# Performance work log

Measured on AMD Instinct MI355X. Metric: run time of the kernel, lower is better.

Reference implementation:

```python
import jax, jax.numpy as jnp
import numpy as np
import math

N_HEADS = 16

def setup_inputs() -> dict:
    key = jax.random.key(0)
    k1, k2, k3 = jax.random.split(key, 3)
    B, S, D = 2, 2048, 1024
    x = jax.random.normal(k1, (B, S, D), dtype=jnp.float32)
    qkv = 0.01 * jax.random.normal(k2, (3 * D, D), dtype=jnp.float32)
    wo = 0.01 * jax.random.normal(k3, (D, D), dtype=jnp.float32)
    return {"x": x, "qkv": qkv, "wo": wo}

def reference(x, qkv, wo):
    B, S, D = x.shape
    H = N_HEADS
    dh = D // H
    QKV = x @ qkv.T                      # [B,S,3D]
    Q, K, V = jnp.split(QKV, 3, axis=-1)
    q = Q.reshape(B, S, H, dh).transpose(0, 2, 1, 3)  # [B,H,S,dh]
    k = K.reshape(B, S, H, dh).transpose(0, 2, 1, 3)
    v = V.reshape(B, S, H, dh).transpose(0, 2, 1, 3)
    scores = jnp.einsum('bhqd,bhkd->bhqk', q, k) / math.sqrt(float(dh))
    # Faithful to original: multiply by lower-triangular mask, then set
    # exact zeros to -inf (masked positions become 0 then -inf).
    mask = jnp.tril(jnp.ones((S, S), dtype=scores.dtype))
    scores = scores * mask[None, None, :, :]
    scores = jnp.where(scores == 0, -jnp.inf, scores)
    attn = jax.nn.softmax(scores, axis=-1)
    out = jnp.einsum('bhqk,bhkd->bhqd', attn, v)       # [B,H,S,dh]
    out = out.transpose(0, 2, 1, 3).reshape(B, S, D)
    return out @ wo.T
```

## Files before the change

kernel.cpp:

```cpp
#include <hip/hip_runtime.h>

typedef unsigned short u16;
typedef unsigned int u32;
typedef __bf16 bf16x8 __attribute__((ext_vector_type(8)));
typedef float f32x4 __attribute__((ext_vector_type(4)));
typedef u16 u16x4 __attribute__((ext_vector_type(4)));
typedef u16 u16x8 __attribute__((ext_vector_type(8)));

#define GL2LDS16(g, l)                                                         \
    __builtin_amdgcn_global_load_lds(                                          \
        (__attribute__((address_space(1))) const void*)(g),                    \
        (__attribute__((address_space(3))) void*)(l), 16, 0, 0)

#define SYNC_VM(n) asm volatile("s_waitcnt vmcnt(" #n ")\ns_barrier" ::: "memory")
#define BAR()      asm volatile("s_barrier" ::: "memory")
#define BAR_DS()   asm volatile("s_waitcnt lgkmcnt(0)\ns_barrier" ::: "memory")

__device__ __forceinline__ u16 f2bf(float f) {
    union { float f; u32 u; } x; x.f = f;
    u32 r = x.u + 0x7FFFu + ((x.u >> 16) & 1u);
    return (u16)(r >> 16);
}

__device__ __forceinline__ u32 pack2bf(float f0, float f1) {
    union { float f; u32 u; } a, b;
    a.f = f0; b.f = f1;
    return __builtin_amdgcn_perm(b.u + 0x8000u, a.u + 0x8000u, 0x07060302u);
}

__device__ __forceinline__ float fast_exp2(float x) {
    float r;
    asm("v_exp_f32 %0, %1" : "=v"(r) : "v"(x));
    return r;
}

__device__ __forceinline__ bf16x8 scale_frag(bf16x8 v) {
#pragma unroll
    for (int i = 0; i < 8; ++i) v[i] = (__bf16)((float)v[i] * 0.1803368801f);
    return v;
}

__global__ __launch_bounds__(256) void convert_all_kernel(const float* __restrict__ x,
                                                          const float* __restrict__ qkv,
                                                          const float* __restrict__ wo,
                                                          u16* __restrict__ out) {
    int i = (blockIdx.x * 256 + threadIdx.x) * 4;
    const float* src;
    int off;
    if (i < 4194304)      { src = x;   off = i; }
    else if (i < 7340032) { src = qkv; off = i - 4194304; }
    else                  { src = wo;  off = i - 7340032; }
    float4 v = *(const float4*)(src + off);
    u16x4 o;
    o.x = f2bf(v.x); o.y = f2bf(v.y); o.z = f2bf(v.z); o.w = f2bf(v.w);
    *(u16x4*)(out + i) = o;
}

template <int TM, bool OUT_BF16, bool FUSE_VT>
__global__ __launch_bounds__(256) void gemm_bt(const u16* __restrict__ A,
                                               const u16* __restrict__ B,
                                               void* __restrict__ Cout,
                                               u16* __restrict__ VtG,
                                               int M, int N, int K) {
    constexpr int MI = TM / 32;
    __shared__ u16 SM[2 * TM * 32 + 2 * 128 * 32];
    u16* Asm = SM;
    u16* Bsm = SM + 2 * TM * 32;
    const int tid = threadIdx.x;
    const int w = tid >> 6, lane = tid & 63, ln = lane & 15, qd = lane >> 4;
    const int wr = w >> 1, wc = w & 1;
    const int m0 = blockIdx.y * TM, n0 = blockIdx.x * 128;

    const int srow = tid >> 2, scol = (tid & 3) * 8;
    const u16* Abase = A + (size_t)(m0 + srow) * K + scol;
    const u16* Bbase = B + (size_t)(n0 + srow) * K + scol;

    f32x4 acc[MI][4] = {};
    const int nsteps = K >> 5;

#pragma unroll
    for (int it = 0; it < TM / 64; ++it)
        GL2LDS16(Abase + (size_t)(it * 64) * K, &Asm[(tid + it * 256) * 8]);
#pragma unroll
    for (int it = 0; it < 2; ++it)
        GL2LDS16(Bbase + (size_t)(it * 64) * K, &Bsm[(tid + it * 256) * 8]);

    for (int s = 0; s < nsteps; ++s) {
        const u16* Ab = &Asm[(s & 1) * TM * 32];
        const u16* Bb = &Bsm[(s & 1) * 128 * 32];
        if (s + 1 < nsteps) {
            const int nk = (s + 1) << 5;
            const int nb = (s + 1) & 1;
#pragma unroll
            for (int it = 0; it < TM / 64; ++it)
                GL2LDS16(Abase + (size_t)(it * 64) * K + nk, &Asm[nb * TM * 32 + (tid + it * 256) * 8]);
#pragma unroll
            for (int it = 0; it < 2; ++it)
                GL2LDS16(Bbase + (size_t)(it * 64) * K + nk, &Bsm[nb * 128 * 32 + (tid + it * 256) * 8]);
            if constexpr (TM == 128) SYNC_VM(4); else SYNC_VM(3);
        } else {
            SYNC_VM(0);
        }

        bf16x8 af[MI], bfr[4];
#pragma unroll
        for (int i = 0; i < MI; ++i)
            af[i] = *(const bf16x8*)&Ab[(wr * (TM / 2) + i * 16 + ln) * 32 + qd * 8];
#pragma unroll
        for (int j = 0; j < 4; ++j)
            bfr[j] = *(const bf16x8*)&Bb[(wc * 64 + j * 16 + ln) * 32 + qd * 8];
        __builtin_amdgcn_s_setprio(1);
#pragma unroll
        for (int i = 0; i < MI; ++i)
#pragma unroll
            for (int j = 0; j < 4; ++j)
                acc[i][j] = __builtin_amdgcn_mfma_f32_16x16x32_bf16(af[i], bfr[j], acc[i][j], 0, 0, 0);
        __builtin_amdgcn_s_setprio(0);
        BAR();
    }

    if constexpr (FUSE_VT) {
        if (n0 >= 2048) {
            const int bq = m0 >> 11;
            BAR_DS();
#pragma unroll
            for (int i = 0; i < MI; ++i)
#pragma unroll
                for (int j = 0; j < 4; ++j) {
                    int col = wc * 64 + j * 16 + ln;
                    int row0 = wr * 64 + i * 16 + qd * 4;
                    int pr = row0 ^ (((col >> 2) & 3) << 4);
                    u16x4 ov;
                    ov.x = f2bf(acc[i][j][0]); ov.y = f2bf(acc[i][j][1]);
                    ov.z = f2bf(acc[i][j][2]); ov.w = f2bf(acc[i][j][3]);
                    *(u16x4*)&SM[col * 128 + pr] = ov;
                }
            BAR_DS();
#pragma unroll
            for (int p = 0; p < 8; ++p) {
                int flat = p * 2048 + tid * 8;
                int colL = flat >> 7, rowL = flat & 127;
                int pr = rowL ^ (((colL >> 2) & 3) << 4);
                u16x8 v = *(const u16x8*)&SM[colL * 128 + pr];
                int d = n0 - 2048 + colL;
                int vrow = (bq * 16 + (d >> 6)) * 64 + (d & 63);
                *(u16x8*)&VtG[(size_t)vrow * 2048 + (m0 & 2047) + rowL] = v;
            }
            return;
        }
    }

#pragma unroll
    for (int i = 0; i < MI; ++i)
#pragma unroll
        for (int j = 0; j < 4; ++j)
#pragma unroll
            for (int r = 0; r < 4; ++r) {
                int row = m0 + wr * (TM / 2) + i * 16 + qd * 4 + r;
                int col = n0 + wc * 64 + j * 16 + ln;
                float v = acc[i][j][r];
                if constexpr (OUT_BF16)
                    ((u16*)Cout)[(size_t)row * N + col] = f2bf(v);
                else
                    ((float*)Cout)[(size_t)row * N + col] = v;
            }
}

__global__ __launch_bounds__(256) void attn_kernel(const u16* __restrict__ QKV,
                                                   const u16* __restrict__ VtG,
                                                   u16* __restrict__ AO) {
    __shared__ u16 Ks[2][64 * 64];
    __shared__ u16 Vts[2][64 * 64];

    const int tid = threadIdx.x;
    const int w = tid >> 6, lane = tid & 63, ln = lane & 15, qd = lane >> 4;
    const int b = blockIdx.z, h = blockIdx.y;
    const int t = blockIdx.x;
    const int tH = 63 - t, tL = t;
    const int tile = (w < 2) ? tH : tL;
    const int myq = tile * 32 + (w & 1) * 16 + ln;
    const int bh = b * 16 + h;
    const int swz = ln & 7;
    const int nchH = (tH >> 1) + 1;
    const int mynch = (tile >> 1) + 1;

    const int sr0 = tid >> 3;
    const int srP = ((sr0 >> 2) & 3) * 8 + ((sr0 >> 4) & 1) * 4 + (sr0 & 3);
    const int sg = (tid & 7) ^ (sr0 & 7);
    const u16* ksrc = QKV + (size_t)(b * 2048 + srP) * 3072 + 1024 + h * 64 + sg * 8;
    const u16* vsrc = VtG + (size_t)(bh * 64 + sr0) * 2048 + sg * 8;

    GL2LDS16(ksrc, &Ks[0][tid * 8]);
    GL2LDS16(ksrc + (size_t)32 * 3072, &Ks[0][tid * 8 + 2048]);
    GL2LDS16(vsrc, &Vts[0][tid * 8]);
    GL2LDS16(vsrc + (size_t)32 * 2048, &Vts[0][tid * 8 + 2048]);

    const u16* qp = QKV + (size_t)(b * 2048 + myq) * 3072 + h * 64;
    bf16x8 qf0 = scale_frag(*(const bf16x8*)(qp + qd * 8));
    bf16x8 qf1 = scale_frag(*(const bf16x8*)(qp + 32 + qd * 8));

    f32x4 o[4] = {};
    float l = 0.f;

    for (int c = 0; c < nchH; ++c) {
        if (c + 1 < nchH) {
            const int k1 = (c + 1) * 64;
            const int nb = (c + 1) & 1;
            GL2LDS16(ksrc + (size_t)k1 * 3072, &Ks[nb][tid * 8]);
            GL2LDS16(ksrc + (size_t)(k1 + 32) * 3072, &Ks[nb][tid * 8 + 2048]);
            GL2LDS16(vsrc + k1, &Vts[nb][tid * 8]);
            GL2LDS16(vsrc + k1 + 32 * 2048, &Vts[nb][tid * 8 + 2048]);
            SYNC_VM(4);
        } else {
            SYNC_VM(0);
        }

        if (c < mynch) {
            const u16* Kb = Ks[c & 1];
            const u16* Vb = Vts[c & 1];

            f32x4 s[4];
            __builtin_amdgcn_s_setprio(1);
#pragma unroll
            for (int kt = 0; kt < 4; ++kt) {
                const u16* kr = Kb + (kt * 16 + ln) * 64;
                bf16x8 kf0 = *(const bf16x8*)(kr + ((qd ^ swz) * 8));
                bf16x8 kf1 = *(const bf16x8*)(kr + (((qd + 4) ^ swz) * 8));
                f32x4 z = {0.f, 0.f, 0.f, 0.f};
                z = __builtin_amdgcn_mfma_f32_16x16x32_bf16(kf0, qf0, z, 0, 0, 0);
                z = __builtin_amdgcn_mfma_f32_16x16x32_bf16(kf1, qf1, z, 0, 0, 0);
                s[kt] = z;
            }
            __builtin_amdgcn_s_setprio(0);

            if (c == mynch - 1) {
#pragma unroll
                for (int kt = 0; kt < 4; ++kt)
#pragma unroll
                    for (int r = 0; r < 4; ++r) {
                        int key = c * 64 + 32 * (kt >> 1) + 8 * qd + 4 * (kt & 1) + r;
                        if (key > myq) s[kt][r] = -1e30f;
                    }
            }

            bf16x8 pf0, pf1;
#pragma unroll
            for (int kt = 0; kt < 4; ++kt)
#pragma unroll
                for (int r = 0; r < 4; ++r) {
                    float p = fast_exp2(s[kt][r]);
                    l += p;
                    if (kt < 2) pf0[(kt & 1) * 4 + r] = (__bf16)p;
                    else        pf1[(kt & 1) * 4 + r] = (__bf16)p;
                }

            __builtin_amdgcn_s_setprio(1);
#pragma unroll
            for (int dt = 0; dt < 4; ++dt) {
                const u16* vr = Vb + (dt * 16 + ln) * 64;
                bf16x8 vf0 = *(const bf16x8*)(vr + ((qd ^ swz) * 8));
                bf16x8 vf1 = *(const bf16x8*)(vr + (((qd + 4) ^ swz) * 8));
                o[dt] = __builtin_amdgcn_mfma_f32_16x16x32_bf16(vf0, pf0, o[dt], 0, 0, 0);
                o[dt] = __builtin_amdgcn_mfma_f32_16x16x32_bf16(vf1, pf1, o[dt], 0, 0, 0);
            }
            __builtin_amdgcn_s_setprio(0);
        }
        BAR();
    }

    l += __shfl_xor(l, 16); l += __shfl_xor(l, 32);
    float inv = 1.0f / l;
#pragma unroll
    for (int dt = 0; dt < 4; ++dt) {
        uint2 ov = {pack2bf(o[dt][0] * inv, o[dt][1] * inv),
                    pack2bf(o[dt][2] * inv, o[dt][3] * inv)};
        *(uint2*)&AO[(size_t)(b * 2048 + myq) * 1024 + h * 64 + dt * 16 + qd * 4] = ov;
    }
}

extern "C" void kernel_launch(void* const* d_in, const int* in_sizes, int n_in,
                              void* d_out, int out_size, void* d_ws, size_t ws_size,
                              hipStream_t stream) {
    const float* x   = (const float*)d_in[0];
    const float* qkv = (const float*)d_in[1];
    const float* wo  = (const float*)d_in[2];
    float* out = (float*)d_out;

    char* ws = (char*)d_ws;
    u16* xb    = (u16*)(ws + 0);
    u16* qkvb  = (u16*)(ws + 8388608);
    u16* wob   = (u16*)(ws + 14680064);
    u16* QKVo  = (u16*)(ws + 16777216);
    u16* AO    = (u16*)(ws + 41943040);
    u16* VtG   = (u16*)(ws + 50331648);

    convert_all_kernel<<<8192, 256, 0, stream>>>(x, qkv, wo, xb);

    gemm_bt<128, true, true><<<dim3(24, 32), 256, 0, stream>>>(xb, qkvb, QKVo, VtG,
                                                               4096, 3072, 1024);

    attn_kernel<<<dim3(32, 16, 2), 256, 0, stream>>>(QKVo, VtG, AO);

    gemm_bt<64, false, false><<<dim3(8, 64), 256, 0, stream>>>(AO, wob, out, nullptr,
                                                               4096, 1024, 1024);
}
```

Baseline: 174.3 us.

## Split heavy-tile key chunks across idle light-tile waves in causal attention

Once the light query tile finishes its causal chunks, its two waves stop idling and each takes half of every remaining 64-key chunk for the heavy tile, while the heavy waves handle the other half. Partial output accumulators and row sums from the light waves are exchanged through LDS scratch, reusing the K/V buffers, and combined before normalisation. This targets the load imbalance between waves, which previously sat at barriers, at the cost of extra registers for a second Q fragment and accumulator plus an LDS reduction at the end.

```diff
diff --git a/kernel.cpp b/kernel.cpp
--- a/kernel.cpp
+++ b/kernel.cpp
@@ -176,13 +176,16 @@
     const int w = tid >> 6, lane = tid & 63, ln = lane & 15, qd = lane >> 4;
     const int b = blockIdx.z, h = blockIdx.y;
     const int t = blockIdx.x;
-    const int tH = 63 - t, tL = t;
-    const int tile = (w < 2) ? tH : tL;
-    const int myq = tile * 32 + (w & 1) * 16 + ln;
+    const int tH = 63 - t;
+    const bool heavy = (w < 2);
+    const int wq = w & 1;
     const int bh = b * 16 + h;
     const int swz = ln & 7;
     const int nchH = (tH >> 1) + 1;
-    const int mynch = (tile >> 1) + 1;
+    const int nchL = (t >> 1) + 1;
+    const int myqH = tH * 32 + wq * 16 + ln;
+    const int myqL = t * 32 + wq * 16 + ln;
+    const int myqA = heavy ? myqH : myqL;
 
     const int sr0 = tid >> 3;
     const int srP = ((sr0 >> 2) & 3) * 8 + ((sr0 >> 4) & 1) * 4 + (sr0 & 3);
@@ -195,12 +198,16 @@
     GL2LDS16(vsrc, &Vts[0][tid * 8]);
     GL2LDS16(vsrc + (size_t)32 * 2048, &Vts[0][tid * 8 + 2048]);
 
-    const u16* qp = QKV + (size_t)(b * 2048 + myq) * 3072 + h * 64;
-    bf16x8 qf0 = scale_frag(*(const bf16x8*)(qp + qd * 8));
-    bf16x8 qf1 = scale_frag(*(const bf16x8*)(qp + 32 + qd * 8));
-
-    f32x4 o[4] = {};
-    float l = 0.f;
+    const u16* qpA = QKV + (size_t)(b * 2048 + myqA) * 3072 + h * 64;
+    const u16* qpH = QKV + (size_t)(b * 2048 + myqH) * 3072 + h * 64;
+    bf16x8 qfa0 = scale_frag(*(const bf16x8*)(qpA + qd * 8));
+    bf16x8 qfa1 = scale_frag(*(const bf16x8*)(qpA + 32 + qd * 8));
+    bf16x8 qfh0 = scale_frag(*(const bf16x8*)(qpH + qd * 8));
+    bf16x8 qfh1 = scale_frag(*(const bf16x8*)(qpH + 32 + qd * 8));
+
+    f32x4 oA[4] = {};
+    f32x4 oH2[4] = {};
+    float lA = 0.f, lH2 = 0.f;
 
     for (int c = 0; c < nchH; ++c) {
         if (c + 1 < nchH) {
@@ -214,11 +221,10 @@
         } else {
             SYNC_VM(0);
         }
-
-        if (c < mynch) {
-            const u16* Kb = Ks[c & 1];
-            const u16* Vb = Vts[c & 1];
-
+        const u16* Kb = Ks[c & 1];
+        const u16* Vb = Vts[c & 1];
+
+        if (c < nchL) {
             f32x4 s[4];
             __builtin_amdgcn_s_setprio(1);
 #pragma unroll
@@ -227,19 +233,19 @@
                 bf16x8 kf0 = *(const bf16x8*)(kr + ((qd ^ swz) * 8));
                 bf16x8 kf1 = *(const bf16x8*)(kr + (((qd + 4) ^ swz) * 8));
                 f32x4 z = {0.f, 0.f, 0.f, 0.f};
-                z = __builtin_amdgcn_mfma_f32_16x16x32_bf16(kf0, qf0, z, 0, 0, 0);
-                z = __builtin_amdgcn_mfma_f32_16x16x32_bf16(kf1, qf1, z, 0, 0, 0);
+                z = __builtin_amdgcn_mfma_f32_16x16x32_bf16(kf0, qfa0, z, 0, 0, 0);
+                z = __builtin_amdgcn_mfma_f32_16x16x32_bf16(kf1, qfa1, z, 0, 0, 0);
                 s[kt] = z;
             }
             __builtin_amdgcn_s_setprio(0);
 
-            if (c == mynch - 1) {
+            if (!heavy && c == nchL - 1) {
 #pragma unroll
                 for (int kt = 0; kt < 4; ++kt)
 #pragma unroll
                     for (int r = 0; r < 4; ++r) {
                         int key = c * 64 + 32 * (kt >> 1) + 8 * qd + 4 * (kt & 1) + r;
-                        if (key > myq) s[kt][r] = -1e30f;
+                        if (key > myqL) s[kt][r] = -1e30f;
                     }
             }
 
@@ -249,7 +255,7 @@
 #pragma unroll
                 for (int r = 0; r < 4; ++r) {
                     float p = fast_exp2(s[kt][r]);
-                    l += p;
+                    lA += p;
                     if (kt < 2) pf0[(kt & 1) * 4 + r] = (__bf16)p;
                     else        pf1[(kt & 1) * 4 + r] = (__bf16)p;
                 }
@@ -260,21 +266,101 @@
                 const u16* vr = Vb + (dt * 16 + ln) * 64;
                 bf16x8 vf0 = *(const bf16x8*)(vr + ((qd ^ swz) * 8));
                 bf16x8 vf1 = *(const bf16x8*)(vr + (((qd + 4) ^ swz) * 8));
-                o[dt] = __builtin_amdgcn_mfma_f32_16x16x32_bf16(vf0, pf0, o[dt], 0, 0, 0);
-                o[dt] = __builtin_amdgcn_mfma_f32_16x16x32_bf16(vf1, pf1, o[dt], 0, 0, 0);
+                oA[dt] = __builtin_amdgcn_mfma_f32_16x16x32_bf16(vf0, pf0, oA[dt], 0, 0, 0);
+                oA[dt] = __builtin_amdgcn_mfma_f32_16x16x32_bf16(vf1, pf1, oA[dt], 0, 0, 0);
             }
             __builtin_amdgcn_s_setprio(0);
+        } else {
+            const int kh = heavy ? 0 : 1;
+            f32x4 s2[2];
+            __builtin_amdgcn_s_setprio(1);
+#pragma unroll
+            for (int ktl = 0; ktl < 2; ++ktl) {
+                const u16* kr = Kb + ((2 * kh + ktl) * 16 + ln) * 64;
+                bf16x8 kf0 = *(const bf16x8*)(kr + ((qd ^ swz) * 8));
+                bf16x8 kf1 = *(const bf16x8*)(kr + (((qd + 4) ^ swz) * 8));
+                f32x4 z = {0.f, 0.f, 0.f, 0.f};
+                z = __builtin_amdgcn_mfma_f32_16x16x32_bf16(kf0, qfh0, z, 0, 0, 0);
+                z = __builtin_amdgcn_mfma_f32_16x16x32_bf16(kf1, qfh1, z, 0, 0, 0);
+                s2[ktl] = z;
+            }
+            __builtin_amdgcn_s_setprio(0);
+
+            if (c == nchH - 1) {
+#pragma unroll
+                for (int ktl = 0; ktl < 2; ++ktl)
+#pragma unroll
+                    for (int r = 0; r < 4; ++r) {
+                        int key = c * 64 + 32 * kh + 8 * qd + 4 * ktl + r;
+                        if (key > myqH) s2[ktl][r] = -1e30f;
+                    }
+            }
+
+            bf16x8 pf;
+            float lacc = 0.f;
+#pragma unroll
+            for (int ktl = 0; ktl < 2; ++ktl)
+#pragma unroll
+                for (int r = 0; r < 4; ++r) {
+                    float p = fast_exp2(s2[ktl][r]);
+                    lacc += p;
+                    pf[ktl * 4 + r] = (__bf16)p;
+                }
+
+            bf16x8 vfh[4];
+#pragma unroll
+            for (int dt = 0; dt < 4; ++dt)
+                vfh[dt] = *(const bf16x8*)&Vb[(dt * 16 + ln) * 64 + (((qd + 4 * kh) ^ swz) * 8)];
+
+            if (heavy) {
+                lA += lacc;
+                __builtin_amdgcn_s_setprio(1);
+#pragma unroll
+                for (int dt = 0; dt < 4; ++dt)
+                    oA[dt] = __builtin_amdgcn_mfma_f32_16x16x32_bf16(vfh[dt], pf, oA[dt], 0, 0, 0);
+                __builtin_amdgcn_s_setprio(0);
+            } else {
+                lH2 += lacc;
+                __builtin_amdgcn_s_setprio(1);
+#pragma unroll
+                for (int dt = 0; dt < 4; ++dt)
+                    oH2[dt] = __builtin_amdgcn_mfma_f32_16x16x32_bf16(vfh[dt], pf, oH2[dt], 0, 0, 0);
+                __builtin_amdgcn_s_setprio(0);
+            }
         }
         BAR();
     }
 
-    l += __shfl_xor(l, 16); l += __shfl_xor(l, 32);
-    float inv = 1.0f / l;
-#pragma unroll
-    for (int dt = 0; dt < 4; ++dt) {
-        uint2 ov = {pack2bf(o[dt][0] * inv, o[dt][1] * inv),
-                    pack2bf(o[dt][2] * inv, o[dt][3] * inv)};
-        *(uint2*)&AO[(size_t)(b * 2048 + myq) * 1024 + h * 64 + dt * 16 + qd * 4] = ov;
+    lA += __shfl_xor(lA, 16); lA += __shfl_xor(lA, 32);
+    lH2 += __shfl_xor(lH2, 16); lH2 += __shfl_xor(lH2, 32);
+    BAR_DS();
+    float* scrO = (float*)&Ks[0][0];
+    float* scrL = (float*)&Vts[0][0];
+    if (!heavy) {
+#pragma unroll
+        for (int dt = 0; dt < 4; ++dt)
+            *(f32x4*)&scrO[(wq * 64 + lane) * 20 + dt * 4] = oH2[dt];
+        scrL[wq * 64 + lane] = lH2;
+    }
+    BAR_DS();
+    if (heavy) {
+        lA += scrL[wq * 64 + lane];
+        float inv = 1.0f / lA;
+#pragma unroll
+        for (int dt = 0; dt < 4; ++dt) {
+            f32x4 s2v = *(const f32x4*)&scrO[(wq * 64 + lane) * 20 + dt * 4];
+            uint2 ov = {pack2bf((oA[dt][0] + s2v[0]) * inv, (oA[dt][1] + s2v[1]) * inv),
+                        pack2bf((oA[dt][2] + s2v[2]) * inv, (oA[dt][3] + s2v[3]) * inv)};
+            *(uint2*)&AO[(size_t)(b * 2048 + myqH) * 1024 + h * 64 + dt * 16 + qd * 4] = ov;
+        }
+    } else {
+        float inv = 1.0f / lA;
+#pragma unroll
+        for (int dt = 0; dt < 4; ++dt) {
+            uint2 ov = {pack2bf(oA[dt][0] * inv, oA[dt][1] * inv),
+                        pack2bf(oA[dt][2] * inv, oA[dt][3] * inv)};
+            *(uint2*)&AO[(size_t)(b * 2048 + myqL) * 1024 + h * 64 + dt * 16 + qd * 4] = ov;
+        }
     }
 }
 
```

New measurement: 193.5 us. 1.11x slower.
